# Kernel tuning notes

Measured on AMD Instinct MI355X. Metric: run time of the kernel, lower is better.

Reference implementation:

```python
import jax, jax.numpy as jnp
import numpy as np

D_MODEL = 768
N_HEAD = 12


def setup_inputs() -> dict:
    key = jax.random.key(0)
    ks = jax.random.split(key, 5)
    B, S, D = 2, 4096, D_MODEL
    scale = 0.02
    return {
        "x": jax.random.normal(ks[0], (B, S, D), dtype=jnp.float32),
        "W_in": jax.random.normal(ks[1], (D, 3 * D), dtype=jnp.float32) * scale,
        "b_in": jax.random.normal(ks[2], (3 * D,), dtype=jnp.float32) * scale,
        "W_out": jax.random.normal(ks[3], (D, D), dtype=jnp.float32) * scale,
        "b_out": jax.random.normal(ks[4], (D,), dtype=jnp.float32) * scale,
    }


def reference(x, W_in, b_in, W_out, b_out):
    B, S, D = x.shape
    H = N_HEAD
    d_head = D // H
    qkv = x @ W_in + b_in                      # [B,S,3D]
    q, k, v = jnp.split(qkv, 3, axis=-1)
    # [B,H,S,d]
    q = q.reshape(B, S, H, d_head).transpose(0, 2, 1, 3)
    k = k.reshape(B, S, H, d_head).transpose(0, 2, 1, 3)
    v = v.reshape(B, S, H, d_head).transpose(0, 2, 1, 3)
    att = jnp.einsum("bhqd,bhkd->bhqk", q, k) * (1.0 / jnp.sqrt(jnp.float32(d_head)))
    causal = jnp.tril(jnp.ones((S, S), dtype=bool))
    att = jnp.where(causal[None, None], att, jnp.float32(-jnp.inf))
    att = jax.nn.softmax(att, axis=-1)
    y = jnp.einsum("bhqk,bhkd->bhqd", att, v)  # [B,H,S,d]
    y = y.transpose(0, 2, 1, 3).reshape(B, S, D)
    return y @ W_out + b_out
```

## Files before the change

kernel.cpp:

```cpp
#include <hip/hip_runtime.h>
#include <hip/hip_bf16.h>


#define D_MODEL 768
#define SEQ 4096
#define NB 2
#define NHEAD 12
#define LDQK 1536

typedef __attribute__((ext_vector_type(8))) short short8;
typedef __attribute__((ext_vector_type(4))) short short4v;
typedef __attribute__((ext_vector_type(4))) float floatx4;

#define SM_C 0.18033688011112042f

#if __has_builtin(__builtin_amdgcn_exp2f)
#define EXP2(x) __builtin_amdgcn_exp2f(x)
#else
#define EXP2(x) __expf((x) * 0.6931471805599453f)
#endif

__device__ inline short fb(float f) {
    union { __hip_bfloat16 h; short s; } cv;
    cv.h = __float2bfloat16(f);
    return cv.s;
}
__device__ inline unsigned pk2(float a, float b) {
    float2 f; f.x = a; f.y = b;
    union { __hip_bfloat162 h; unsigned u; } cv;
    cv.h = __float22bfloat162_rn(f);
    return cv.u;
}
__device__ inline void gload16(const void* g, void* l) {
    __builtin_amdgcn_global_load_lds(
        (const __attribute__((address_space(1))) unsigned int*)g,
        (__attribute__((address_space(3))) unsigned int*)l, 16, 0, 0);
}

__global__ __launch_bounds__(256) void convert_bf16(const float* __restrict__ src,
                                                    short* __restrict__ dst, size_t n) {
    size_t i = ((size_t)blockIdx.x * 256 + threadIdx.x) * 8;
    if (i >= n) return;
    float4 f0 = *(const float4*)(src + i);
    float4 f1 = *(const float4*)(src + i + 4);
    uint4 u = {pk2(f0.x, f0.y), pk2(f0.z, f0.w), pk2(f1.x, f1.y), pk2(f1.z, f1.w)};
    *(uint4*)(dst + i) = u;
}

__global__ __launch_bounds__(256) void transpose_bf16(const float* __restrict__ W,
                                                      short* __restrict__ Wt,
                                                      int K, int N) {
    __shared__ short t[32][33];
    const int n0 = blockIdx.x * 32, k0 = blockIdx.y * 32;
    const int tx = threadIdx.x, ty = threadIdx.y;
#pragma unroll
    for (int j = 0; j < 4; ++j)
        t[ty + j * 8][tx] = fb(W[(size_t)(k0 + ty + j * 8) * N + n0 + tx]);
    __syncthreads();
#pragma unroll
    for (int j = 0; j < 4; ++j)
        Wt[(size_t)(n0 + ty + j * 8) * K + k0 + tx] = t[tx][ty + j * 8];
}

__global__ __launch_bounds__(256) void gemm_qkv128(const short* __restrict__ A,
                                                   const short* __restrict__ Bt,
                                                   const float* __restrict__ bias,
                                                   short* __restrict__ qkw,
                                                   short* __restrict__ vtw) {
    const int K = D_MODEL;
    __shared__ short As[128][32];
    __shared__ short Bs[128][32];
    const int tid = threadIdx.x, lane = tid & 63, w = tid >> 6;
    const int wr = w >> 1, wc = w & 1;
    const int lo = lane & 15, hi = lane >> 4;
    const int m0 = blockIdx.y * 128, n0 = blockIdx.x * 128;
    const int lr = lane >> 2, lc = (lane & 3) * 8;

    floatx4 acc[4][4] = {};
    const short* Ag = A  + (size_t)(m0 + w * 16 + lr) * K + lc;
    const short* Bg = Bt + (size_t)(n0 + w * 16 + lr) * K + lc;

    for (int k0 = 0; k0 < K; k0 += 32) {
        __syncthreads();
        gload16(Ag + k0,                  &As[w * 16][0]);
        gload16(Ag + k0 + (size_t)64 * K, &As[64 + w * 16][0]);
        gload16(Bg + k0,                  &Bs[w * 16][0]);
        gload16(Bg + k0 + (size_t)64 * K, &Bs[64 + w * 16][0]);
        __syncthreads();
        short8 a[4], bf[4];
#pragma unroll
        for (int m = 0; m < 4; ++m) a[m] = *(const short8*)&As[wr * 64 + m * 16 + lo][hi * 8];
#pragma unroll
        for (int n = 0; n < 4; ++n) bf[n] = *(const short8*)&Bs[wc * 64 + n * 16 + lo][hi * 8];
#pragma unroll
        for (int m = 0; m < 4; ++m)
#pragma unroll
            for (int n = 0; n < 4; ++n)
                acc[m][n] = __builtin_amdgcn_mfma_f32_16x16x32_bf16(a[m], bf[n], acc[m][n], 0, 0, 0);
    }

#pragma unroll
    for (int m = 0; m < 4; ++m)
#pragma unroll
        for (int n = 0; n < 4; ++n) {
            int col  = n0 + wc * 64 + n * 16 + lo;
            int row0 = m0 + wr * 64 + m * 16 + hi * 4;
            float bv = bias[col];
            if (col < LDQK) {
#pragma unroll
                for (int r = 0; r < 4; ++r)
                    qkw[(size_t)(row0 + r) * LDQK + col] = fb(acc[m][n][r] + bv);
            } else {
                int vcol = col - LDQK;
                int hh = vcol >> 6, dh = vcol & 63;
                int bb = row0 >> 12, s = row0 & 4095;
                uint2 u = {pk2(acc[m][n][0] + bv, acc[m][n][1] + bv),
                           pk2(acc[m][n][2] + bv, acc[m][n][3] + bv)};
                *(uint2*)&vtw[(((size_t)bb * NHEAD + hh) * 64 + dh) * SEQ + s] = u;
            }
        }
}

__global__ __launch_bounds__(256) void gemm_out128(const short* __restrict__ A,
                                                   const short* __restrict__ Bt,
                                                   const float* __restrict__ bias,
                                                   float* __restrict__ C) {
    const int K = D_MODEL, N = D_MODEL;
    __shared__ short As[128][32];
    __shared__ short Bs[128][32];
    const int tid = threadIdx.x, lane = tid & 63, w = tid >> 6;
    const int wr = w >> 1, wc = w & 1;
    const int lo = lane & 15, hi = lane >> 4;
    const int m0 = blockIdx.y * 128, n0 = blockIdx.x * 128;
    const int lr = lane >> 2, lc = (lane & 3) * 8;

    floatx4 acc[4][4] = {};
    const short* Ag = A  + (size_t)(m0 + w * 16 + lr) * K + lc;
    const short* Bg = Bt + (size_t)(n0 + w * 16 + lr) * K + lc;

    for (int k0 = 0; k0 < K; k0 += 32) {
        __syncthreads();
        gload16(Ag + k0,                  &As[w * 16][0]);
        gload16(Ag + k0 + (size_t)64 * K, &As[64 + w * 16][0]);
        gload16(Bg + k0,                  &Bs[w * 16][0]);
        gload16(Bg + k0 + (size_t)64 * K, &Bs[64 + w * 16][0]);
        __syncthreads();
        short8 a[4], bf[4];
#pragma unroll
        for (int m = 0; m < 4; ++m) a[m] = *(const short8*)&As[wr * 64 + m * 16 + lo][hi * 8];
#pragma unroll
        for (int n = 0; n < 4; ++n) bf[n] = *(const short8*)&Bs[wc * 64 + n * 16 + lo][hi * 8];
#pragma unroll
        for (int m = 0; m < 4; ++m)
#pragma unroll
            for (int n = 0; n < 4; ++n)
                acc[m][n] = __builtin_amdgcn_mfma_f32_16x16x32_bf16(a[m], bf[n], acc[m][n], 0, 0, 0);
    }

#pragma unroll
    for (int m = 0; m < 4; ++m)
#pragma unroll
        for (int n = 0; n < 4; ++n) {
            int col  = n0 + wc * 64 + n * 16 + lo;
            int row0 = m0 + wr * 64 + m * 16 + hi * 4;
            float bv = bias[col];
#pragma unroll
            for (int r = 0; r < 4; ++r)
                C[(size_t)(row0 + r) * N + col] = acc[m][n][r] + bv;
        }
}

__global__ __launch_bounds__(256) void attn_k(const short* __restrict__ qk,
                                              const short* __restrict__ vt,
                                              short* __restrict__ y) {
    const int ip = blockIdx.x, h = blockIdx.y, b = blockIdx.z;
    const int tid = threadIdx.x, lane = tid & 63, w = tid >> 6;
    const int lo = lane & 15, hi = lane >> 4;

    __shared__ alignas(16) short Ks[64 * 64];
    __shared__ alignas(16) short Vs[64 * 64];
    __shared__ alignas(16) short Ps[4 * 16 * 64];

    const short* qbase = qk + (size_t)b * SEQ * LDQK;
    const short* kbase = qbase + D_MODEL;
    const short* vbase = vt + ((size_t)b * NHEAD + h) * 64 * SEQ;

    const int skey = tid >> 2, sdc = tid & 3;
    const int sdim = tid >> 2, skg = tid & 3;

    short* kcommit0 = &Ks[skey * 64 + (((sdc * 2)    ) ^ (skey & 7)) * 8];
    short* kcommit1 = &Ks[skey * 64 + (((sdc * 2) + 1) ^ (skey & 7)) * 8];
    short* vcommit0 = &Vs[sdim * 64 + (((skg * 2)    ) ^ (sdim & 7)) * 8];
    short* vcommit1 = &Vs[sdim * 64 + (((skg * 2) + 1) ^ (sdim & 7)) * 8];
    unsigned* pwbase = (unsigned*)&Ps[w * 1024];

    for (int t = 0; t < 2; ++t) {
        const int qt = t ? ip : 63 - ip;
        const int q0 = qt * 64;

        short8 qf[2];
        {
            const short* qrow = qbase + (size_t)(q0 + w * 16 + lo) * LDQK + h * 64;
            qf[0] = *(const short8*)(qrow + hi * 8);
            qf[1] = *(const short8*)(qrow + 32 + hi * 8);
        }

        floatx4 o[4] = {};
        float mrun = -1e30f, mC = -1e28f, lrun = 0.0f;
        float sc4[4];

        const short* kptr = kbase + (size_t)skey * LDQK + h * 64 + sdc * 16;
        const short* vptr = vbase + (size_t)sdim * SEQ + skg * 16;
        short8 kpre[2], vpre[2];
        kpre[0] = *(const short8*)kptr;
        kpre[1] = *(const short8*)(kptr + 8);
        vpre[0] = *(const short8*)vptr;
        vpre[1] = *(const short8*)(vptr + 8);

        auto tile_body = [&](bool diag) {
            floatx4 sT[4];
            __builtin_amdgcn_s_setprio(1);
#pragma unroll
            for (int c = 0; c < 4; ++c) {
                floatx4 acc = {};
#pragma unroll
                for (int kc = 0; kc < 2; ++kc) {
                    short8 kf = *(const short8*)&Ks[(c * 16 + lo) * 64 + ((kc * 4 + hi) ^ (lo & 7)) * 8];
                    acc = __builtin_amdgcn_mfma_f32_16x16x32_bf16(kf, qf[kc], acc, 0, 0, 0);
                }
                sT[c] = acc;
            }
            __builtin_amdgcn_s_setprio(0);

            const int qin = w * 16 + lo;
            if (diag) {
#pragma unroll
                for (int c = 0; c < 4; ++c)
#pragma unroll
                    for (int r = 0; r < 4; ++r)
                        if ((c * 16 + hi * 4 + r) > qin) sT[c][r] = -1e30f;
            }
            float mc[4];
#pragma unroll
            for (int c = 0; c < 4; ++c)
                mc[c] = fmaxf(fmaxf(sT[c][0], sT[c][1]), fmaxf(sT[c][2], sT[c][3]));
            float mx = fmaxf(fmaxf(mc[0], mc[1]), fmaxf(mc[2], mc[3]));
            mx = fmaxf(mx, __shfl_xor(mx, 16, 64));
            mx = fmaxf(mx, __shfl_xor(mx, 32, 64));

            float lsc = 1.0f;
            if (__any(mx - mrun > 64.0f)) {
                float mnew = fmaxf(mrun, mx);
                float sc = EXP2((mrun - mnew) * SM_C);
                mrun = mnew;
                mC = mnew * SM_C;
                lsc = sc;
#pragma unroll
                for (int r = 0; r < 4; ++r) sc4[r] = __shfl(sc, hi * 4 + r, 16);
#pragma unroll
                for (int dc = 0; dc < 4; ++dc)
#pragma unroll
                    for (int r = 0; r < 4; ++r) o[dc][r] *= sc4[r];
            }

            float p[4][4];
            float rs = 0.0f;
#pragma unroll
            for (int c = 0; c < 4; ++c)
#pragma unroll
                for (int r = 0; r < 4; ++r) {
                    float e = EXP2(__builtin_fmaf(sT[c][r], SM_C, -mC));
                    p[c][r] = e;
                    rs += e;
                }
            rs += __shfl_xor(rs, 16, 64);
            rs += __shfl_xor(rs, 32, 64);
            lrun = __builtin_fmaf(lrun, lsc, rs);

#pragma unroll
            for (int c = 0; c < 4; ++c) {
                uint2 word = {pk2(p[c][0], p[c][1]), pk2(p[c][2], p[c][3])};
                *(uint2*)(pwbase + ((lo * 64 + (((c * 4 + hi) ^ (lo & 14)) * 4)) >> 1)) = word;
            }
            asm volatile("s_waitcnt lgkmcnt(0)" ::: "memory");

            __builtin_amdgcn_s_setprio(1);
#pragma unroll
            for (int kc = 0; kc < 2; ++kc) {
                short8 af = *(const short8*)&Ps[w * 1024 + lo * 64 + ((kc * 8 + hi * 2) ^ (lo & 14)) * 4];
#pragma unroll
                for (int dc = 0; dc < 4; ++dc) {
                    short8 vf = *(const short8*)&Vs[(dc * 16 + lo) * 64 + ((kc * 4 + hi) ^ (lo & 7)) * 8];
                    o[dc] = __builtin_amdgcn_mfma_f32_16x16x32_bf16(af, vf, o[dc], 0, 0, 0);
                }
            }
            __builtin_amdgcn_s_setprio(0);
        };

        for (int kb = 0; kb < qt; ++kb) {
            __syncthreads();
            *(short8*)kcommit0 = kpre[0];
            *(short8*)kcommit1 = kpre[1];
            *(short8*)vcommit0 = vpre[0];
            *(short8*)vcommit1 = vpre[1];
            __syncthreads();
            kptr += (size_t)64 * LDQK;
            vptr += 64;
            kpre[0] = *(const short8*)kptr;
            kpre[1] = *(const short8*)(kptr + 8);
            vpre[0] = *(const short8*)vptr;
            vpre[1] = *(const short8*)(vptr + 8);
            tile_body(false);
        }
        __syncthreads();
        *(short8*)kcommit0 = kpre[0];
        *(short8*)kcommit1 = kpre[1];
        *(short8*)vcommit0 = vpre[0];
        *(short8*)vcommit1 = vpre[1];
        __syncthreads();
        tile_body(true);

#pragma unroll
        for (int r = 0; r < 4; ++r) sc4[r] = __shfl(lrun, hi * 4 + r, 16);
#pragma unroll
        for (int r = 0; r < 4; ++r) {
            float inv = 1.0f / sc4[r];
            int row = q0 + w * 16 + hi * 4 + r;
            short* dst = y + ((size_t)b * SEQ + row) * D_MODEL + h * 64;
#pragma unroll
            for (int dc = 0; dc < 4; ++dc) dst[dc * 16 + lo] = fb(o[dc][r] * inv);
        }
    }
}

extern "C" void kernel_launch(void* const* d_in, const int* in_sizes, int n_in,
                              void* d_out, int out_size, void* d_ws, size_t ws_size,
                              hipStream_t stream) {
    (void)in_sizes; (void)n_in; (void)out_size; (void)ws_size;
    const float* x     = (const float*)d_in[0];
    const float* W_in  = (const float*)d_in[1];
    const float* b_in  = (const float*)d_in[2];
    const float* W_out = (const float*)d_in[3];
    const float* b_out = (const float*)d_in[4];
    float* out = (float*)d_out;

    const int M = NB * SEQ;
    char* p = (char*)d_ws;
    short* xbf   = (short*)p; p += (size_t)M * D_MODEL * 2;
    short* wtin  = (short*)p; p += (size_t)3 * D_MODEL * D_MODEL * 2;
    short* wtout = (short*)p; p += (size_t)D_MODEL * D_MODEL * 2;
    short* qkw   = (short*)p; p += (size_t)M * LDQK * 2;
    short* vtw   = (short*)p; p += (size_t)NB * NHEAD * 64 * SEQ * 2;
    short* yw    = (short*)p;

    convert_bf16<<<dim3((unsigned)((size_t)M * D_MODEL / 8 / 256)), 256, 0, stream>>>(
        x, xbf, (size_t)M * D_MODEL);
    transpose_bf16<<<dim3(3 * D_MODEL / 32, D_MODEL / 32), dim3(32, 8), 0, stream>>>(
        W_in, wtin, D_MODEL, 3 * D_MODEL);
    transpose_bf16<<<dim3(D_MODEL / 32, D_MODEL / 32), dim3(32, 8), 0, stream>>>(
        W_out, wtout, D_MODEL, D_MODEL);
    gemm_qkv128<<<dim3(3 * D_MODEL / 128, M / 128), 256, 0, stream>>>(
        xbf, wtin, b_in, qkw, vtw);
    attn_k<<<dim3(SEQ / 128, NHEAD, NB), 256, 0, stream>>>(qkw, vtw, yw);
    gemm_out128<<<dim3(D_MODEL / 128, M / 128), 256, 0, stream>>>(yw, wtout, b_out, out);
}
```

Measured before the change: 194.6 us.

## Restructure attention to 2-wave blocks with 32 query rows each and double-buffered K/V

The attention kernel moves from 4 waves with 16 query rows each to 2 waves with 32 rows each, so each K/V fragment read from LDS feeds two MFMAs. K/V tiles are now double-buffered in shared memory, which removes one barrier per key block and overlaps the commit of the next tile with compute on the current one. The cost is higher register pressure, plus fewer waves per block, mitigated by launch_bounds(128,2).

```diff
diff --git a/kernel.cpp b/kernel.cpp
--- a/kernel.cpp
+++ b/kernel.cpp
@@ -9,7 +9,6 @@
 #define LDQK 1536
 
 typedef __attribute__((ext_vector_type(8))) short short8;
-typedef __attribute__((ext_vector_type(4))) short short4v;
 typedef __attribute__((ext_vector_type(4))) float floatx4;
 
 #define SM_C 0.18033688011112042f
@@ -170,165 +169,195 @@
         }
 }
 
-__global__ __launch_bounds__(256) void attn_k(const short* __restrict__ qk,
-                                              const short* __restrict__ vt,
-                                              short* __restrict__ y) {
+__global__ __launch_bounds__(128, 2) void attn_k(const short* __restrict__ qk,
+                                                 const short* __restrict__ vt,
+                                                 short* __restrict__ y) {
     const int ip = blockIdx.x, h = blockIdx.y, b = blockIdx.z;
     const int tid = threadIdx.x, lane = tid & 63, w = tid >> 6;
     const int lo = lane & 15, hi = lane >> 4;
 
-    __shared__ alignas(16) short Ks[64 * 64];
-    __shared__ alignas(16) short Vs[64 * 64];
-    __shared__ alignas(16) short Ps[4 * 16 * 64];
+    __shared__ alignas(16) short Ks[2][64 * 64];
+    __shared__ alignas(16) short Vs[2][64 * 64];
+    __shared__ alignas(16) short Ps[2 * 2 * 1024];
 
     const short* qbase = qk + (size_t)b * SEQ * LDQK;
     const short* kbase = qbase + D_MODEL;
     const short* vbase = vt + ((size_t)b * NHEAD + h) * 64 * SEQ;
 
-    const int skey = tid >> 2, sdc = tid & 3;
-    const int sdim = tid >> 2, skg = tid & 3;
-
-    short* kcommit0 = &Ks[skey * 64 + (((sdc * 2)    ) ^ (skey & 7)) * 8];
-    short* kcommit1 = &Ks[skey * 64 + (((sdc * 2) + 1) ^ (skey & 7)) * 8];
-    short* vcommit0 = &Vs[sdim * 64 + (((skg * 2)    ) ^ (sdim & 7)) * 8];
-    short* vcommit1 = &Vs[sdim * 64 + (((skg * 2) + 1) ^ (sdim & 7)) * 8];
-    unsigned* pwbase = (unsigned*)&Ps[w * 1024];
+    const int srow = tid >> 1, shalf = tid & 1;
+    int cof[4];
+#pragma unroll
+    for (int j = 0; j < 4; ++j)
+        cof[j] = srow * 64 + ((shalf * 4 + j) ^ (srow & 7)) * 8;
 
     for (int t = 0; t < 2; ++t) {
         const int qt = t ? ip : 63 - ip;
         const int q0 = qt * 64;
-
-        short8 qf[2];
-        {
-            const short* qrow = qbase + (size_t)(q0 + w * 16 + lo) * LDQK + h * 64;
-            qf[0] = *(const short8*)(qrow + hi * 8);
-            qf[1] = *(const short8*)(qrow + 32 + hi * 8);
-        }
-
-        floatx4 o[4] = {};
-        float mrun = -1e30f, mC = -1e28f, lrun = 0.0f;
-        float sc4[4];
-
-        const short* kptr = kbase + (size_t)skey * LDQK + h * 64 + sdc * 16;
-        const short* vptr = vbase + (size_t)sdim * SEQ + skg * 16;
-        short8 kpre[2], vpre[2];
-        kpre[0] = *(const short8*)kptr;
-        kpre[1] = *(const short8*)(kptr + 8);
-        vpre[0] = *(const short8*)vptr;
-        vpre[1] = *(const short8*)(vptr + 8);
-
-        auto tile_body = [&](bool diag) {
-            floatx4 sT[4];
+        const int nkb = qt + 1;
+
+        short8 qf[2][2];
+#pragma unroll
+        for (int mq = 0; mq < 2; ++mq) {
+            const short* qrow = qbase + (size_t)(q0 + w * 32 + mq * 16 + lo) * LDQK + h * 64;
+            qf[mq][0] = *(const short8*)(qrow + hi * 8);
+            qf[mq][1] = *(const short8*)(qrow + 32 + hi * 8);
+        }
+
+        floatx4 o[2][4] = {};
+        float mrun[2] = {-1e30f, -1e30f}, mCv[2] = {-1e28f, -1e28f}, lrun[2] = {0.0f, 0.0f};
+
+        const short* kptr = kbase + (size_t)srow * LDQK + h * 64 + shalf * 32;
+        const short* vptr = vbase + (size_t)srow * SEQ + shalf * 32;
+        short8 kpre[4], vpre[4];
+#pragma unroll
+        for (int j = 0; j < 4; ++j) {
+            kpre[j] = *(const short8*)(kptr + j * 8);
+            vpre[j] = *(const short8*)(vptr + j * 8);
+        }
+#pragma unroll
+        for (int j = 0; j < 4; ++j) {
+            *(short8*)&Ks[0][cof[j]] = kpre[j];
+            *(short8*)&Vs[0][cof[j]] = vpre[j];
+        }
+        if (nkb > 1) {
+            kptr += (size_t)64 * LDQK;
+            vptr += 64;
+#pragma unroll
+            for (int j = 0; j < 4; ++j) {
+                kpre[j] = *(const short8*)(kptr + j * 8);
+                vpre[j] = *(const short8*)(vptr + j * 8);
+            }
+        }
+        __syncthreads();
+
+        int c = 0;
+        auto tile_body = [&](int cb, bool diag) {
+            const short* Kb = Ks[cb];
+            const short* Vb = Vs[cb];
+            floatx4 sT[2][4];
             __builtin_amdgcn_s_setprio(1);
 #pragma unroll
-            for (int c = 0; c < 4; ++c) {
-                floatx4 acc = {};
+            for (int cc = 0; cc < 4; ++cc) {
+                floatx4 a0 = {}, a1 = {};
 #pragma unroll
                 for (int kc = 0; kc < 2; ++kc) {
-                    short8 kf = *(const short8*)&Ks[(c * 16 + lo) * 64 + ((kc * 4 + hi) ^ (lo & 7)) * 8];
-                    acc = __builtin_amdgcn_mfma_f32_16x16x32_bf16(kf, qf[kc], acc, 0, 0, 0);
-                }
-                sT[c] = acc;
+                    short8 kf = *(const short8*)&Kb[(cc * 16 + lo) * 64 + ((kc * 4 + hi) ^ (lo & 7)) * 8];
+                    a0 = __builtin_amdgcn_mfma_f32_16x16x32_bf16(kf, qf[0][kc], a0, 0, 0, 0);
+                    a1 = __builtin_amdgcn_mfma_f32_16x16x32_bf16(kf, qf[1][kc], a1, 0, 0, 0);
+                }
+                sT[0][cc] = a0;
+                sT[1][cc] = a1;
             }
             __builtin_amdgcn_s_setprio(0);
 
-            const int qin = w * 16 + lo;
-            if (diag) {
-#pragma unroll
-                for (int c = 0; c < 4; ++c)
-#pragma unroll
-                    for (int r = 0; r < 4; ++r)
-                        if ((c * 16 + hi * 4 + r) > qin) sT[c][r] = -1e30f;
-            }
-            float mc[4];
-#pragma unroll
-            for (int c = 0; c < 4; ++c)
-                mc[c] = fmaxf(fmaxf(sT[c][0], sT[c][1]), fmaxf(sT[c][2], sT[c][3]));
-            float mx = fmaxf(fmaxf(mc[0], mc[1]), fmaxf(mc[2], mc[3]));
-            mx = fmaxf(mx, __shfl_xor(mx, 16, 64));
-            mx = fmaxf(mx, __shfl_xor(mx, 32, 64));
-
-            float lsc = 1.0f;
-            if (__any(mx - mrun > 64.0f)) {
-                float mnew = fmaxf(mrun, mx);
-                float sc = EXP2((mrun - mnew) * SM_C);
-                mrun = mnew;
-                mC = mnew * SM_C;
-                lsc = sc;
-#pragma unroll
-                for (int r = 0; r < 4; ++r) sc4[r] = __shfl(sc, hi * 4 + r, 16);
-#pragma unroll
-                for (int dc = 0; dc < 4; ++dc)
-#pragma unroll
-                    for (int r = 0; r < 4; ++r) o[dc][r] *= sc4[r];
-            }
-
-            float p[4][4];
-            float rs = 0.0f;
-#pragma unroll
-            for (int c = 0; c < 4; ++c)
-#pragma unroll
-                for (int r = 0; r < 4; ++r) {
-                    float e = EXP2(__builtin_fmaf(sT[c][r], SM_C, -mC));
-                    p[c][r] = e;
-                    rs += e;
-                }
-            rs += __shfl_xor(rs, 16, 64);
-            rs += __shfl_xor(rs, 32, 64);
-            lrun = __builtin_fmaf(lrun, lsc, rs);
-
-#pragma unroll
-            for (int c = 0; c < 4; ++c) {
-                uint2 word = {pk2(p[c][0], p[c][1]), pk2(p[c][2], p[c][3])};
-                *(uint2*)(pwbase + ((lo * 64 + (((c * 4 + hi) ^ (lo & 14)) * 4)) >> 1)) = word;
+#pragma unroll
+            for (int mq = 0; mq < 2; ++mq) {
+                const int qin = w * 32 + mq * 16 + lo;
+                if (diag) {
+#pragma unroll
+                    for (int cc = 0; cc < 4; ++cc)
+#pragma unroll
+                        for (int r = 0; r < 4; ++r)
+                            if ((cc * 16 + hi * 4 + r) > qin) sT[mq][cc][r] = -1e30f;
+                }
+                float mc[4];
+#pragma unroll
+                for (int cc = 0; cc < 4; ++cc)
+                    mc[cc] = fmaxf(fmaxf(sT[mq][cc][0], sT[mq][cc][1]),
+                                   fmaxf(sT[mq][cc][2], sT[mq][cc][3]));
+                float mx = fmaxf(fmaxf(mc[0], mc[1]), fmaxf(mc[2], mc[3]));
+                mx = fmaxf(mx, __shfl_xor(mx, 16, 64));
+                mx = fmaxf(mx, __shfl_xor(mx, 32, 64));
+
+                float lsc = 1.0f;
+                if (__any(mx - mrun[mq] > 64.0f)) {
+                    float mnew = fmaxf(mrun[mq], mx);
+                    float sc = EXP2((mrun[mq] - mnew) * SM_C);
+                    mrun[mq] = mnew;
+                    mCv[mq] = mnew * SM_C;
+                    lsc = sc;
+                    float sc4[4];
+#pragma unroll
+                    for (int r = 0; r < 4; ++r) sc4[r] = __shfl(sc, hi * 4 + r, 16);
+#pragma unroll
+                    for (int dc = 0; dc < 4; ++dc)
+#pragma unroll
+                        for (int r = 0; r < 4; ++r) o[mq][dc][r] *= sc4[r];
+                }
+
+                float rs = 0.0f;
+#pragma unroll
+                for (int cc = 0; cc < 4; ++cc)
+#pragma unroll
+                    for (int r = 0; r < 4; ++r) {
+                        float e = EXP2(__builtin_fmaf(sT[mq][cc][r], SM_C, -mCv[mq]));
+                        sT[mq][cc][r] = e;
+                        rs += e;
+                    }
+                rs += __shfl_xor(rs, 16, 64);
+                rs += __shfl_xor(rs, 32, 64);
+                lrun[mq] = __builtin_fmaf(lrun[mq], lsc, rs);
+
+                unsigned* pw = (unsigned*)&Ps[(w * 2 + mq) * 1024];
+#pragma unroll
+                for (int cc = 0; cc < 4; ++cc) {
+                    uint2 word = {pk2(sT[mq][cc][0], sT[mq][cc][1]),
+                                  pk2(sT[mq][cc][2], sT[mq][cc][3])};
+                    *(uint2*)(pw + ((lo * 64 + (((cc * 4 + hi) ^ (lo & 14)) * 4)) >> 1)) = word;
+                }
             }
             asm volatile("s_waitcnt lgkmcnt(0)" ::: "memory");
 
             __builtin_amdgcn_s_setprio(1);
 #pragma unroll
             for (int kc = 0; kc < 2; ++kc) {
-                short8 af = *(const short8*)&Ps[w * 1024 + lo * 64 + ((kc * 8 + hi * 2) ^ (lo & 14)) * 4];
+                short8 af0 = *(const short8*)&Ps[(w * 2 + 0) * 1024 + lo * 64 + ((kc * 8 + hi * 2) ^ (lo & 14)) * 4];
+                short8 af1 = *(const short8*)&Ps[(w * 2 + 1) * 1024 + lo * 64 + ((kc * 8 + hi * 2) ^ (lo & 14)) * 4];
 #pragma unroll
                 for (int dc = 0; dc < 4; ++dc) {
-                    short8 vf = *(const short8*)&Vs[(dc * 16 + lo) * 64 + ((kc * 4 + hi) ^ (lo & 7)) * 8];
-                    o[dc] = __builtin_amdgcn_mfma_f32_16x16x32_bf16(af, vf, o[dc], 0, 0, 0);
+                    short8 vf = *(const short8*)&Vb[(dc * 16 + lo) * 64 + ((kc * 4 + hi) ^ (lo & 7)) * 8];
+                    o[0][dc] = __builtin_amdgcn_mfma_f32_16x16x32_bf16(af0, vf, o[0][dc], 0, 0, 0);
+                    o[1][dc] = __builtin_amdgcn_mfma_f32_16x16x32_bf16(af1, vf, o[1][dc], 0, 0, 0);
                 }
             }
             __builtin_amdgcn_s_setprio(0);
         };
 
-        for (int kb = 0; kb < qt; ++kb) {
+        for (int kb = 0; kb < nkb; ++kb) {
+            if (kb + 1 < nkb) {
+#pragma unroll
+                for (int j = 0; j < 4; ++j) {
+                    *(short8*)&Ks[c ^ 1][cof[j]] = kpre[j];
+                    *(short8*)&Vs[c ^ 1][cof[j]] = vpre[j];
+                }
+                if (kb + 2 < nkb) {
+                    kptr += (size_t)64 * LDQK;
+                    vptr += 64;
+#pragma unroll
+                    for (int j = 0; j < 4; ++j) {
+                        kpre[j] = *(const short8*)(kptr + j * 8);
+                        vpre[j] = *(const short8*)(vptr + j * 8);
+                    }
+                }
+            }
+            tile_body(c, kb == nkb - 1);
             __syncthreads();
-            *(short8*)kcommit0 = kpre[0];
-            *(short8*)kcommit1 = kpre[1];
-            *(short8*)vcommit0 = vpre[0];
-            *(short8*)vcommit1 = vpre[1];
-            __syncthreads();
-            kptr += (size_t)64 * LDQK;
-            vptr += 64;
-            kpre[0] = *(const short8*)kptr;
-            kpre[1] = *(const short8*)(kptr + 8);
-            vpre[0] = *(const short8*)vptr;
-            vpre[1] = *(const short8*)(vptr + 8);
-            tile_body(false);
-        }
-        __syncthreads();
-        *(short8*)kcommit0 = kpre[0];
-        *(short8*)kcommit1 = kpre[1];
-        *(short8*)vcommit0 = vpre[0];
-        *(short8*)vcommit1 = vpre[1];
-        __syncthreads();
-        tile_body(true);
-
-#pragma unroll
-        for (int r = 0; r < 4; ++r) sc4[r] = __shfl(lrun, hi * 4 + r, 16);
-#pragma unroll
-        for (int r = 0; r < 4; ++r) {
-            float inv = 1.0f / sc4[r];
-            int row = q0 + w * 16 + hi * 4 + r;
-            short* dst = y + ((size_t)b * SEQ + row) * D_MODEL + h * 64;
-#pragma unroll
-            for (int dc = 0; dc < 4; ++dc) dst[dc * 16 + lo] = fb(o[dc][r] * inv);
+            c ^= 1;
+        }
+
+#pragma unroll
+        for (int mq = 0; mq < 2; ++mq) {
+            float l4[4];
+#pragma unroll
+            for (int r = 0; r < 4; ++r) l4[r] = __shfl(lrun[mq], hi * 4 + r, 16);
+#pragma unroll
+            for (int r = 0; r < 4; ++r) {
+                float inv = 1.0f / l4[r];
+                int row = q0 + w * 32 + mq * 16 + hi * 4 + r;
+                short* dst = y + ((size_t)b * SEQ + row) * D_MODEL + h * 64;
+#pragma unroll
+                for (int dc = 0; dc < 4; ++dc) dst[dc * 16 + lo] = fb(o[mq][dc][r] * inv);
+            }
         }
     }
 }
@@ -361,6 +390,6 @@
         W_out, wtout, D_MODEL, D_MODEL);
     gemm_qkv128<<<dim3(3 * D_MODEL / 128, M / 128), 256, 0, stream>>>(
         xbf, wtin, b_in, qkw, vtw);
-    attn_k<<<dim3(SEQ / 128, NHEAD, NB), 256, 0, stream>>>(qkw, vtw, yw);
+    attn_k<<<dim3(SEQ / 128, NHEAD, NB), 128, 0, stream>>>(qkw, vtw, yw);
     gemm_out128<<<dim3(D_MODEL / 128, M / 128), 256, 0, stream>>>(yw, wtout, b_out, out);
 }
```

New measurement: 233.0 us. +19.8%, slower.

## Process 128-key tiles per attention iteration instead of 64

Applied to the files above, without the earlier changes.

The attention kernel now stages 128 keys of K and V per iteration, halving the number of loop trips, barriers and online-softmax rescale checks per query tile. The LDS swizzles for K, V and P are reworked for the wider tiles, and the diagonal mask is computed from global key and query indices because the last 128-key block can straddle the diagonal. Launch bounds now request three blocks per CU. The cost is more registers and LDS per block, plus some wasted masked work on the final tile for even-numbered query tiles.

```diff
diff --git a/kernel.cpp b/kernel.cpp
--- a/kernel.cpp
+++ b/kernel.cpp
@@ -9,7 +9,6 @@
 #define LDQK 1536
 
 typedef __attribute__((ext_vector_type(8))) short short8;
-typedef __attribute__((ext_vector_type(4))) short short4v;
 typedef __attribute__((ext_vector_type(4))) float floatx4;
 
 #define SM_C 0.18033688011112042f
@@ -170,33 +169,35 @@
         }
 }
 
-__global__ __launch_bounds__(256) void attn_k(const short* __restrict__ qk,
-                                              const short* __restrict__ vt,
-                                              short* __restrict__ y) {
+__global__ __launch_bounds__(256, 3) void attn_k(const short* __restrict__ qk,
+                                                 const short* __restrict__ vt,
+                                                 short* __restrict__ y) {
     const int ip = blockIdx.x, h = blockIdx.y, b = blockIdx.z;
     const int tid = threadIdx.x, lane = tid & 63, w = tid >> 6;
     const int lo = lane & 15, hi = lane >> 4;
 
-    __shared__ alignas(16) short Ks[64 * 64];
-    __shared__ alignas(16) short Vs[64 * 64];
-    __shared__ alignas(16) short Ps[4 * 16 * 64];
+    __shared__ alignas(16) short Ks[128 * 64];
+    __shared__ alignas(16) short Vs[64 * 128];
+    __shared__ alignas(16) short Ps[4 * 16 * 128];
 
     const short* qbase = qk + (size_t)b * SEQ * LDQK;
     const short* kbase = qbase + D_MODEL;
     const short* vbase = vt + ((size_t)b * NHEAD + h) * 64 * SEQ;
 
-    const int skey = tid >> 2, sdc = tid & 3;
-    const int sdim = tid >> 2, skg = tid & 3;
-
-    short* kcommit0 = &Ks[skey * 64 + (((sdc * 2)    ) ^ (skey & 7)) * 8];
-    short* kcommit1 = &Ks[skey * 64 + (((sdc * 2) + 1) ^ (skey & 7)) * 8];
-    short* vcommit0 = &Vs[sdim * 64 + (((skg * 2)    ) ^ (sdim & 7)) * 8];
-    short* vcommit1 = &Vs[sdim * 64 + (((skg * 2) + 1) ^ (sdim & 7)) * 8];
-    unsigned* pwbase = (unsigned*)&Ps[w * 1024];
+    const int skey = tid >> 1, sdh = tid & 1;
+    const int sdim = tid >> 2, skq = tid & 3;
+    int kcof[4], vcof[4];
+#pragma unroll
+    for (int j = 0; j < 4; ++j) {
+        kcof[j] = skey * 64 + ((sdh * 4 + j) ^ (skey & 7)) * 8;
+        vcof[j] = sdim * 128 + ((skq * 4 + j) ^ (sdim & 15)) * 8;
+    }
+    unsigned* pwbase = (unsigned*)&Ps[w * 2048];
 
     for (int t = 0; t < 2; ++t) {
         const int qt = t ? ip : 63 - ip;
         const int q0 = qt * 64;
+        const int n128 = (qt + 2) >> 1;
 
         short8 qf[2];
         {
@@ -209,42 +210,45 @@
         float mrun = -1e30f, mC = -1e28f, lrun = 0.0f;
         float sc4[4];
 
-        const short* kptr = kbase + (size_t)skey * LDQK + h * 64 + sdc * 16;
-        const short* vptr = vbase + (size_t)sdim * SEQ + skg * 16;
-        short8 kpre[2], vpre[2];
-        kpre[0] = *(const short8*)kptr;
-        kpre[1] = *(const short8*)(kptr + 8);
-        vpre[0] = *(const short8*)vptr;
-        vpre[1] = *(const short8*)(vptr + 8);
-
-        auto tile_body = [&](bool diag) {
-            floatx4 sT[4];
+        const short* kptr = kbase + (size_t)skey * LDQK + h * 64 + sdh * 32;
+        const short* vptr = vbase + (size_t)sdim * SEQ + skq * 32;
+        short8 kpre[4], vpre[4];
+#pragma unroll
+        for (int j = 0; j < 4; ++j) {
+            kpre[j] = *(const short8*)(kptr + j * 8);
+            vpre[j] = *(const short8*)(vptr + j * 8);
+        }
+
+        auto tile_body = [&](int kb, bool diag) {
+            floatx4 sT[8];
             __builtin_amdgcn_s_setprio(1);
 #pragma unroll
-            for (int c = 0; c < 4; ++c) {
+            for (int cc = 0; cc < 8; ++cc) {
                 floatx4 acc = {};
 #pragma unroll
                 for (int kc = 0; kc < 2; ++kc) {
-                    short8 kf = *(const short8*)&Ks[(c * 16 + lo) * 64 + ((kc * 4 + hi) ^ (lo & 7)) * 8];
+                    short8 kf = *(const short8*)&Ks[(cc * 16 + lo) * 64 + ((kc * 4 + hi) ^ (lo & 7)) * 8];
                     acc = __builtin_amdgcn_mfma_f32_16x16x32_bf16(kf, qf[kc], acc, 0, 0, 0);
                 }
-                sT[c] = acc;
+                sT[cc] = acc;
             }
             __builtin_amdgcn_s_setprio(0);
 
-            const int qin = w * 16 + lo;
             if (diag) {
-#pragma unroll
-                for (int c = 0; c < 4; ++c)
+                const int qg = q0 + w * 16 + lo;
+                const int kb0 = kb * 128;
+#pragma unroll
+                for (int cc = 0; cc < 8; ++cc)
 #pragma unroll
                     for (int r = 0; r < 4; ++r)
-                        if ((c * 16 + hi * 4 + r) > qin) sT[c][r] = -1e30f;
-            }
-            float mc[4];
-#pragma unroll
-            for (int c = 0; c < 4; ++c)
-                mc[c] = fmaxf(fmaxf(sT[c][0], sT[c][1]), fmaxf(sT[c][2], sT[c][3]));
-            float mx = fmaxf(fmaxf(mc[0], mc[1]), fmaxf(mc[2], mc[3]));
+                        if ((kb0 + cc * 16 + hi * 4 + r) > qg) sT[cc][r] = -1e30f;
+            }
+            float mc[8];
+#pragma unroll
+            for (int cc = 0; cc < 8; ++cc)
+                mc[cc] = fmaxf(fmaxf(sT[cc][0], sT[cc][1]), fmaxf(sT[cc][2], sT[cc][3]));
+            float mx = fmaxf(fmaxf(fmaxf(mc[0], mc[1]), fmaxf(mc[2], mc[3])),
+                             fmaxf(fmaxf(mc[4], mc[5]), fmaxf(mc[6], mc[7])));
             mx = fmaxf(mx, __shfl_xor(mx, 16, 64));
             mx = fmaxf(mx, __shfl_xor(mx, 32, 64));
 
@@ -263,14 +267,13 @@
                     for (int r = 0; r < 4; ++r) o[dc][r] *= sc4[r];
             }
 
-            float p[4][4];
             float rs = 0.0f;
 #pragma unroll
-            for (int c = 0; c < 4; ++c)
+            for (int cc = 0; cc < 8; ++cc)
 #pragma unroll
                 for (int r = 0; r < 4; ++r) {
-                    float e = EXP2(__builtin_fmaf(sT[c][r], SM_C, -mC));
-                    p[c][r] = e;
+                    float e = EXP2(__builtin_fmaf(sT[cc][r], SM_C, -mC));
+                    sT[cc][r] = e;
                     rs += e;
                 }
             rs += __shfl_xor(rs, 16, 64);
@@ -278,47 +281,51 @@
             lrun = __builtin_fmaf(lrun, lsc, rs);
 
 #pragma unroll
-            for (int c = 0; c < 4; ++c) {
-                uint2 word = {pk2(p[c][0], p[c][1]), pk2(p[c][2], p[c][3])};
-                *(uint2*)(pwbase + ((lo * 64 + (((c * 4 + hi) ^ (lo & 14)) * 4)) >> 1)) = word;
+            for (int cc = 0; cc < 8; ++cc) {
+                uint2 word = {pk2(sT[cc][0], sT[cc][1]), pk2(sT[cc][2], sT[cc][3])};
+                *(uint2*)(pwbase + lo * 64 + (((cc * 2 + (hi >> 1)) ^ (lo & 15)) * 4) + (hi & 1) * 2) = word;
             }
             asm volatile("s_waitcnt lgkmcnt(0)" ::: "memory");
 
             __builtin_amdgcn_s_setprio(1);
 #pragma unroll
-            for (int kc = 0; kc < 2; ++kc) {
-                short8 af = *(const short8*)&Ps[w * 1024 + lo * 64 + ((kc * 8 + hi * 2) ^ (lo & 14)) * 4];
+            for (int kc = 0; kc < 4; ++kc) {
+                short8 af = *(const short8*)&Ps[w * 2048 + lo * 128 + ((kc * 4 + hi) ^ (lo & 15)) * 8];
 #pragma unroll
                 for (int dc = 0; dc < 4; ++dc) {
-                    short8 vf = *(const short8*)&Vs[(dc * 16 + lo) * 64 + ((kc * 4 + hi) ^ (lo & 7)) * 8];
+                    short8 vf = *(const short8*)&Vs[(dc * 16 + lo) * 128 + ((kc * 4 + hi) ^ (lo & 15)) * 8];
                     o[dc] = __builtin_amdgcn_mfma_f32_16x16x32_bf16(af, vf, o[dc], 0, 0, 0);
                 }
             }
             __builtin_amdgcn_s_setprio(0);
         };
 
-        for (int kb = 0; kb < qt; ++kb) {
+        for (int kb = 0; kb < n128 - 1; ++kb) {
             __syncthreads();
-            *(short8*)kcommit0 = kpre[0];
-            *(short8*)kcommit1 = kpre[1];
-            *(short8*)vcommit0 = vpre[0];
-            *(short8*)vcommit1 = vpre[1];
+#pragma unroll
+            for (int j = 0; j < 4; ++j) {
+                *(short8*)&Ks[kcof[j]] = kpre[j];
+                *(short8*)&Vs[vcof[j]] = vpre[j];
+            }
             __syncthreads();
-            kptr += (size_t)64 * LDQK;
-            vptr += 64;
-            kpre[0] = *(const short8*)kptr;
-            kpre[1] = *(const short8*)(kptr + 8);
-            vpre[0] = *(const short8*)vptr;
-            vpre[1] = *(const short8*)(vptr + 8);
-            tile_body(false);
-        }
-        __syncthreads();
-        *(short8*)kcommit0 = kpre[0];
-        *(short8*)kcommit1 = kpre[1];
-        *(short8*)vcommit0 = vpre[0];
-        *(short8*)vcommit1 = vpre[1];
-        __syncthreads();
-        tile_body(true);
+            kptr += (size_t)128 * LDQK;
+            vptr += 128;
+#pragma unroll
+            for (int j = 0; j < 4; ++j) {
+                kpre[j] = *(const short8*)(kptr + j * 8);
+                vpre[j] = *(const short8*)(vptr + j * 8);
+            }
+            tile_body(kb, false);
+        }
+        __syncthreads();
+#pragma unroll
+        for (int j = 0; j < 4; ++j) {
+            *(short8*)&Ks[kcof[j]] = kpre[j];
+            *(short8*)&Vs[vcof[j]] = vpre[j];
+        }
+        __syncthreads();
+        tile_body(n128 - 1, true);
+        __syncthreads();
 
 #pragma unroll
         for (int r = 0; r < 4; ++r) sc4[r] = __shfl(lrun, hi * 4 + r, 16);
```

After: 201.8 us. +3.7%, slower.
